# Kernel tuning notes

Hardware: AMD Instinct MI355X
Metric: run time of the kernel (lower is better)

The kernel has to match this reference:

```python
import jax, jax.numpy as jnp
import numpy as np

N = 200000   # active voxels
G = 128      # dense grid extent per axis
C = 128      # hidden channels
IN_C = 1
TEMB = 6
K = 27       # 3x3x3 kernel offsets


def _build_neighbors():
    # Sample N unique voxel coordinates in a G^3 grid and build the 27-offset
    # rulebook: neighbor_idx[k, i] = index of voxel at coord[i] + offset[k],
    # or N (sentinel -> zero-padded feature row) if inactive.
    rng = np.random.default_rng(0)
    lin = np.sort(rng.choice(G ** 3, size=N, replace=False)).astype(np.int64)
    x, r = lin // (G * G), lin % (G * G)
    y, z = r // G, r % G
    nidx = np.full((K, N), N, dtype=np.int32)
    k = 0
    for dx in (-1, 0, 1):
        for dy in (-1, 0, 1):
            for dz in (-1, 0, 1):
                nx, ny, nz = x + dx, y + dy, z + dz
                valid = (nx >= 0) & (nx < G) & (ny >= 0) & (ny < G) & (nz >= 0) & (nz < G)
                key = nx * (G * G) + ny * G + nz
                pos = np.searchsorted(lin, key)
                posc = np.clip(pos, 0, N - 1)
                found = valid & (lin[posc] == key)
                nidx[k] = np.where(found, posc, N).astype(np.int32)
                k += 1
    return jnp.asarray(nidx)


def setup_inputs() -> dict:
    key = jax.random.key(0)
    ks = jax.random.split(key, 8)
    s = jnp.float32(0.05)
    return {
        "features": jax.random.normal(ks[0], (N, IN_C), jnp.float32),
        "t": jax.random.randint(ks[1], (N,), 0, 1000, jnp.int32),
        "neighbor_idx": _build_neighbors(),
        "W1": jax.random.normal(ks[2], (K, IN_C + TEMB, C), jnp.float32) * s,
        "b1": jnp.zeros((C,), jnp.float32),
        "W2": jax.random.normal(ks[3], (K, C, C), jnp.float32) * s,
        "b2": jnp.zeros((C,), jnp.float32),
        "W3": jax.random.normal(ks[4], (C, C), jnp.float32) * s,
        "b3": jnp.zeros((C,), jnp.float32),
        "W4": jax.random.normal(ks[5], (C, 1), jnp.float32) * s,
        "b4": jnp.zeros((1,), jnp.float32),
    }


def _sinusoidal(t, dim):
    half = dim // 2
    freqs = (2.0 ** jnp.arange(half, dtype=jnp.float32)) * jnp.pi  # 2^k * pi
    ang = t.astype(jnp.float32)[:, None] * freqs[None, :]
    return jnp.concatenate([jnp.sin(ang), jnp.cos(ang)], -1)  # [N, dim]


def _sparse_conv3(x, W, b, nidx):
    # Submanifold sparse 3x3x3 conv: for each of 27 offsets, gather neighbor
    # features (zero row for missing) and accumulate a [Cin,Cout] matmul.
    xpad = jnp.concatenate([x, jnp.zeros((1, x.shape[1]), x.dtype)], 0)  # sentinel row
    acc0 = jnp.zeros((x.shape[0], W.shape[-1]), x.dtype)

    def step(acc, kw):
        idx, Wk = kw
        return acc + xpad[idx] @ Wk, None

    acc, _ = jax.lax.scan(step, acc0, (nidx, W))
    return acc + b


def reference(features, t, neighbor_idx, W1, b1, W2, b2, W3, b3, W4, b4):
    # time-embedding concat  [N, 1+6]
    x = jnp.concatenate([features, _sinusoidal(t, TEMB)], -1)
    # SparseConv3d(k=3) + Dropout(eval: identity) + SiLU
    h = jax.nn.silu(_sparse_conv3(x, W1, b1, neighbor_idx))
    h = jax.nn.silu(_sparse_conv3(h, W2, b2, neighbor_idx))
    # SparseConv3d(k=1) + SiLU  == pointwise matmul
    h = jax.nn.silu(h @ W3 + b3)
    # final 1x1 conv to out_channels=1
    return h @ W4 + b4
```

## Files before the change

kernel.cpp:

```cpp
#include <hip/hip_runtime.h>
#include <math.h>

#define N_VOX 200000
#define CCH   128
#define KOFF  27

typedef __attribute__((ext_vector_type(8))) short bf16x8;
typedef __attribute__((ext_vector_type(4))) float f32x4;

__device__ __forceinline__ float silu_f(float x) {
    return x / (1.0f + expf(-x));
}
__device__ __forceinline__ unsigned short f2bf(float x) {
    unsigned int u = __float_as_uint(x);
    u = (u + 0x7FFFu + ((u >> 16) & 1u)) >> 16;
    return (unsigned short)u;
}
__device__ __forceinline__ int xcd_swz(int orig, int nwg) {
    int q = nwg >> 3, r = nwg & 7;
    int xcd = orig & 7, pos = orig >> 3;
    return (xcd < r ? xcd * (q + 1) : r * (q + 1) + (xcd - r) * q) + pos;
}
__device__ __forceinline__ void gload_lds16(const void* g, void* l) {
    __builtin_amdgcn_global_load_lds(
        (const __attribute__((address_space(1))) unsigned int*)g,
        (__attribute__((address_space(3))) unsigned int*)l, 16, 0, 0);
}

__global__ void embed_kernel(const float* __restrict__ feat,
                             const int* __restrict__ t,
                             unsigned short* __restrict__ xeb) {
    int i = blockIdx.x * blockDim.x + threadIdx.x;
    if (i > N_VOX) return;
    union { unsigned short u[8]; int4 v; } o;
    if (i == N_VOX) {
        o.v = make_int4(0, 0, 0, 0);
    } else {
        o.u[0] = f2bf(feat[i]);
        float tf = (float)t[i];
#pragma unroll
        for (int kk = 0; kk < 3; ++kk) {
            float freq = (float)M_PI * (float)(1 << kk);
            float ang = tf * freq;
            o.u[1 + kk] = f2bf(sinf(ang));
            o.u[4 + kk] = f2bf(cosf(ang));
        }
        o.u[7] = 0;
    }
    *(int4*)(xeb + (size_t)i * 8) = o.v;
}

__global__ void convert_w1(const float* __restrict__ W1,
                           unsigned short* __restrict__ W1f) {
    int g = blockIdx.x * 256 + threadIdx.x;
    if (g >= 7 * 8 * 64) return;
    int l = g & 63;
    int rest = g >> 6;
    int nf = rest & 7;
    int kk = rest >> 3;
    int o = kk * 4 + (l >> 4);
    int co = nf * 16 + (l & 15);
    union { unsigned short u[8]; int4 v; } out;
#pragma unroll
    for (int j = 0; j < 8; ++j) {
        float w = 0.f;
        if (o < KOFF && j < 7) w = W1[((size_t)o * 7 + j) * CCH + co];
        out.u[j] = f2bf(w);
    }
    *(int4*)(W1f + (size_t)g * 8) = out.v;
}

__global__ void convert_w2(const float* __restrict__ W2,
                           unsigned short* __restrict__ W2f) {
    int g = blockIdx.x * 256 + threadIdx.x;
    int l = g & 63;
    int rest = g >> 6;
    int nf = rest & 7;
    int kkk = rest >> 3;
    int k = kkk >> 2, kk = kkk & 3;
    int ci0 = kk * 32 + (l >> 4) * 8;
    int co = nf * 16 + (l & 15);
    union { unsigned short u[8]; int4 v; } out;
#pragma unroll
    for (int j = 0; j < 8; ++j)
        out.u[j] = f2bf(W2[((size_t)k * CCH + ci0 + j) * CCH + co]);
    *(int4*)(W2f + (size_t)g * 8) = out.v;
}

__global__ void convert_w3(const float* __restrict__ W3,
                           unsigned short* __restrict__ W3f) {
    int g = blockIdx.x * 256 + threadIdx.x;
    if (g >= 4 * 8 * 64) return;
    int l = g & 63;
    int rest = g >> 6;
    int nf = rest & 7;
    int kk = rest >> 3;
    int ci0 = kk * 32 + (l >> 4) * 8;
    int co = nf * 16 + (l & 15);
    union { unsigned short u[8]; int4 v; } out;
#pragma unroll
    for (int j = 0; j < 8; ++j)
        out.u[j] = f2bf(W3[(size_t)(ci0 + j) * CCH + co]);
    *(int4*)(W3f + (size_t)g * 8) = out.v;
}

__global__ __launch_bounds__(256) void conv1_mfma(
    const unsigned short* __restrict__ xeb, const int* __restrict__ nidx,
    const unsigned short* __restrict__ W1f, const float* __restrict__ b1,
    unsigned short* __restrict__ h1b) {
    __shared__ int4 bufmem[2048];
    __shared__ int idxAll[128 * 28];

    int tid = threadIdx.x;
    int l = tid & 63, w = tid >> 6;
    int mw = w >> 1, nwv = w & 1;
    int wg = xcd_swz(blockIdx.x, gridDim.x);
    int v0 = wg * 128;

    for (int g = tid; g < KOFF * 128; g += 256) {
        int k = g >> 7, vi = g & 127;
        int v = v0 + vi;
        idxAll[vi * 28 + k] = (v < N_VOX) ? nidx[(size_t)k * N_VOX + v] : N_VOX;
    }
    if (tid < 128) idxAll[tid * 28 + 27] = N_VOX;
    __syncthreads();

    f32x4 acc[4][4];
#pragma unroll
    for (int m = 0; m < 4; ++m)
#pragma unroll
        for (int n = 0; n < 4; ++n) acc[m][n] = (f32x4)0.f;

    {
        int4 g0[2]; int rr[2], cc[2];
#pragma unroll
        for (int u = 0; u < 2; ++u) {
            int q = u * 256 + tid;
            int r = q >> 2, oo = q & 3;
            int idx = idxAll[r * 28 + oo];
            g0[u] = *(const int4*)(xeb + (size_t)idx * 8);
            rr[u] = r; cc[u] = oo ^ (r & 3);
        }
#pragma unroll
        for (int u = 0; u < 2; ++u) bufmem[rr[u] * 5 + cc[u]] = g0[u];
    }
    __syncthreads();

    for (int kk = 0; kk < 7; ++kk) {
        int cur = kk & 1;
        int4 gg[2]; int rr[2], cc[2];
        if (kk < 6) {
#pragma unroll
            for (int u = 0; u < 2; ++u) {
                int q = u * 256 + tid;
                int r = q >> 2, oo = q & 3;
                int idx = idxAll[r * 28 + (kk + 1) * 4 + oo];
                gg[u] = *(const int4*)(xeb + (size_t)idx * 8);
                rr[u] = r; cc[u] = oo ^ (r & 3);
            }
        }
        bf16x8 a[4], b[4];
#pragma unroll
        for (int n = 0; n < 4; ++n) {
            int nf = nwv * 4 + n;
            b[n] = *(const bf16x8*)(W1f + ((size_t)(kk * 8 + nf) * 64 + l) * 8);
        }
#pragma unroll
        for (int m = 0; m < 4; ++m) {
            int r = mw * 64 + m * 16 + (l & 15);
            int c = l >> 4;
            a[m] = *(const bf16x8*)&bufmem[cur * 640 + r * 5 + (c ^ (r & 3))];
        }
#pragma unroll
        for (int m = 0; m < 4; ++m)
#pragma unroll
            for (int n = 0; n < 4; ++n)
                acc[m][n] = __builtin_amdgcn_mfma_f32_16x16x32_bf16(
                    a[m], b[n], acc[m][n], 0, 0, 0);
        if (kk < 6) {
#pragma unroll
            for (int u = 0; u < 2; ++u)
                bufmem[(cur ^ 1) * 640 + rr[u] * 5 + cc[u]] = gg[u];
        }
        __syncthreads();
    }

    float bias[4];
#pragma unroll
    for (int n = 0; n < 4; ++n) bias[n] = b1[nwv * 64 + n * 16 + (l & 15)];
    unsigned short* H16 = (unsigned short*)bufmem;
#pragma unroll
    for (int m = 0; m < 4; ++m) {
        int rbase = mw * 64 + m * 16 + (l >> 4) * 4;
#pragma unroll
        for (int n = 0; n < 4; ++n) {
            int ch = nwv * 64 + n * 16 + (l & 15);
            int c = ch >> 3;
            f32x4 d = acc[m][n];
#pragma unroll
            for (int ri = 0; ri < 4; ++ri) {
                int r = rbase + ri;
                int s = (c & 8) | ((c & 7) ^ (r & 7));
                H16[r * 128 + s * 8 + (ch & 7)] = f2bf(silu_f(d[ri] + bias[n]));
            }
        }
    }
    __syncthreads();
#pragma unroll
    for (int u = 0; u < 8; ++u) {
        int q = u * 256 + tid;
        int r = q >> 4, s = q & 15;
        int c = (s & 8) | ((s & 7) ^ (r & 7));
        int v = v0 + r;
        if (v < N_VOX)
            *(int4*)(h1b + (size_t)v * CCH + c * 8) = bufmem[r * 16 + s];
    }
    if (blockIdx.x == 0 && tid < 16)
        *(int4*)(h1b + (size_t)N_VOX * CCH + tid * 8) = make_int4(0, 0, 0, 0);
}

#define STAGE3(bufsel, kq) {                                               \
    int _c = (w << 2) + (l >> 4);                                          \
    _Pragma("unroll") for (int _u = 0; _u < 8; ++_u) {                     \
        int _r = _u * 16 + (l & 15);                                       \
        int _idx = idxAll[(kq) * 128 + _r];                                \
        gload_lds16((const char*)h1b + ((size_t)_idx << 8) + (_c << 4),    \
                    (void*)&Abuf[bufsel][_u * 256 + tid]);                 \
    }                                                                      \
}

#define LOADB2(dst, kq, kh) {                                              \
    const unsigned short* _wb = W2f + (size_t)(kq) * 16384;                \
    _Pragma("unroll") for (int _j = 0; _j < 2; ++_j)                       \
        _Pragma("unroll") for (int _n = 0; _n < 4; ++_n)                   \
            dst[_j][_n] = *(const bf16x8*)(_wb +                           \
                ((size_t)(((kh)*2 + _j) * 8 + nwv * 4 + _n) * 64 + l) * 8);\
}

#define MPH(cur, kk, br) {                                                 \
    bf16x8 _a[4];                                                          \
    _Pragma("unroll") for (int _m = 0; _m < 4; ++_m)                       \
        _a[_m] = *(const bf16x8*)                                          \
            &Abuf[cur][(((mw * 4 + _m) * 4 + (kk)) << 6) + l];             \
    _Pragma("unroll") for (int _m = 0; _m < 4; ++_m)                       \
        _Pragma("unroll") for (int _n = 0; _n < 4; ++_n)                   \
            acc[_m][_n] = __builtin_amdgcn_mfma_f32_16x16x32_bf16(         \
                _a[_m], br[_n], acc[_m][_n], 0, 0, 0);                     \
}

#define STEP(KQ, BCUR, BNXT) {                                             \
    int _cur = (KQ) & 1, _nxt = _cur ^ 1;                                  \
    STAGE3(_nxt, (KQ) + 1);                                                \
    __builtin_amdgcn_sched_barrier(0);                                     \
    bf16x8 b23[2][4];                                                      \
    LOADB2(b23, (KQ), 1);                                                  \
    LOADB2(BNXT, (KQ) + 1, 0);                                             \
    __builtin_amdgcn_sched_barrier(0);                                     \
    MPH(_cur, 0, BCUR[0]);                                                 \
    MPH(_cur, 1, BCUR[1]);                                                 \
    MPH(_cur, 2, b23[0]);                                                  \
    MPH(_cur, 3, b23[1]);                                                  \
    asm volatile("s_waitcnt vmcnt(8)" ::: "memory");                       \
    __builtin_amdgcn_s_barrier();                                          \
}

__global__ __launch_bounds__(256, 2) void conv2_mfma(
    const unsigned short* __restrict__ h1b, const int* __restrict__ nidx,
    const unsigned short* __restrict__ W2f, const float* __restrict__ b2,
    const unsigned short* __restrict__ W3f, const float* __restrict__ b3,
    const float* __restrict__ W4, const float* __restrict__ b4,
    float* __restrict__ out) {
    __shared__ int4 Abuf[2][2048];
    __shared__ int idxAll[KOFF * 128];

    int tid = threadIdx.x;
    int l = tid & 63, w = tid >> 6;
    int mw = w >> 1, nwv = w & 1;
    int wg = xcd_swz(blockIdx.x, gridDim.x);
    int v0 = wg * 128;

    for (int g = tid; g < KOFF * 128; g += 256) {
        int k = g >> 7, vi = g & 127;
        int v = v0 + vi;
        idxAll[k * 128 + vi] = (v < N_VOX) ? nidx[(size_t)k * N_VOX + v] : N_VOX;
    }
    __syncthreads();

    f32x4 acc[4][4];
#pragma unroll
    for (int m = 0; m < 4; ++m)
#pragma unroll
        for (int n = 0; n < 4; ++n) acc[m][n] = (f32x4)0.f;

    bf16x8 bE[2][4], bO[2][4];

    STAGE3(0, 0);
    __builtin_amdgcn_sched_barrier(0);
    LOADB2(bE, 0, 0);
    __builtin_amdgcn_sched_barrier(0);
    asm volatile("s_waitcnt vmcnt(8)" ::: "memory");
    __builtin_amdgcn_s_barrier();

    for (int kp = 0; kp < 26; kp += 2) {
        STEP(kp, bE, bO);
        STEP(kp + 1, bO, bE);
    }
    {
        bf16x8 b23[2][4];
        LOADB2(b23, 26, 1);
        MPH(0, 0, bE[0]);
        MPH(0, 1, bE[1]);
        MPH(0, 2, b23[0]);
        MPH(0, 3, b23[1]);
    }
    __syncthreads();

    float bias2[4];
#pragma unroll
    for (int n = 0; n < 4; ++n) bias2[n] = b2[nwv * 64 + n * 16 + (l & 15)];
    unsigned short* H16 = (unsigned short*)&Abuf[0][0];
#pragma unroll
    for (int m = 0; m < 4; ++m) {
        int rbase = mw * 64 + m * 16 + (l >> 4) * 4;
#pragma unroll
        for (int n = 0; n < 4; ++n) {
            int ch = nwv * 64 + n * 16 + (l & 15);
            int c = ch >> 3;
            f32x4 d = acc[m][n];
#pragma unroll
            for (int ri = 0; ri < 4; ++ri) {
                int r = rbase + ri;
                int s = (c & 8) | ((c & 7) ^ (r & 7));
                H16[r * 128 + s * 8 + (ch & 7)] = f2bf(silu_f(d[ri] + bias2[n]));
            }
        }
    }
    __syncthreads();

    f32x4 p[4][4];
#pragma unroll
    for (int m = 0; m < 4; ++m)
#pragma unroll
        for (int n = 0; n < 4; ++n) p[m][n] = (f32x4)0.f;
#pragma unroll
    for (int kk = 0; kk < 4; ++kk) {
        bf16x8 a[4], b[4];
#pragma unroll
        for (int n = 0; n < 4; ++n) {
            int nf = nwv * 4 + n;
            b[n] = *(const bf16x8*)(W3f + ((size_t)(kk * 8 + nf) * 64 + l) * 8);
        }
#pragma unroll
        for (int m = 0; m < 4; ++m) {
            int r = mw * 64 + m * 16 + (l & 15);
            int c = kk * 4 + (l >> 4);
            int s = (c & 8) | ((c & 7) ^ (r & 7));
            a[m] = *(const bf16x8*)&H16[r * 128 + s * 8];
        }
#pragma unroll
        for (int m = 0; m < 4; ++m)
#pragma unroll
            for (int n = 0; n < 4; ++n)
                p[m][n] = __builtin_amdgcn_mfma_f32_16x16x32_bf16(
                    a[m], b[n], p[m][n], 0, 0, 0);
    }

    float w4v[4], b3v[4];
#pragma unroll
    for (int n = 0; n < 4; ++n) {
        int ch = nwv * 64 + n * 16 + (l & 15);
        w4v[n] = W4[ch];
        b3v[n] = b3[ch];
    }
    float* Osum = (float*)idxAll;
#pragma unroll
    for (int m = 0; m < 4; ++m) {
        float po[4] = {0.f, 0.f, 0.f, 0.f};
#pragma unroll
        for (int n = 0; n < 4; ++n) {
            f32x4 d = p[m][n];
#pragma unroll
            for (int ri = 0; ri < 4; ++ri)
                po[ri] += silu_f(d[ri] + b3v[n]) * w4v[n];
        }
#pragma unroll
        for (int off = 1; off < 16; off <<= 1)
#pragma unroll
            for (int ri = 0; ri < 4; ++ri)
                po[ri] += __shfl_xor(po[ri], off, 64);
        if ((l & 15) == 0) {
            int rbase = mw * 64 + m * 16 + (l >> 4) * 4;
#pragma unroll
            for (int ri = 0; ri < 4; ++ri)
                Osum[nwv * 128 + rbase + ri] = po[ri];
        }
    }
    __syncthreads();
    if (tid < 128) {
        int v = v0 + tid;
        if (v < N_VOX) out[v] = Osum[tid] + Osum[128 + tid] + b4[0];
    }
}

extern "C" void kernel_launch(void* const* d_in, const int* in_sizes, int n_in,
                              void* d_out, int out_size, void* d_ws,
                              size_t ws_size, hipStream_t stream) {
    const float* feat = (const float*)d_in[0];
    const int* t      = (const int*)d_in[1];
    const int* nidx   = (const int*)d_in[2];
    const float* W1   = (const float*)d_in[3];
    const float* b1   = (const float*)d_in[4];
    const float* W2   = (const float*)d_in[5];
    const float* b2   = (const float*)d_in[6];
    const float* W3   = (const float*)d_in[7];
    const float* b3   = (const float*)d_in[8];
    const float* W4   = (const float*)d_in[9];
    const float* b4   = (const float*)d_in[10];
    float* out = (float*)d_out;

    char* ws = (char*)d_ws;
    size_t off = 0;
    unsigned short* xeb = (unsigned short*)(ws + off);
    off += ((size_t)(N_VOX + 1) * 8 * 2 + 255) & ~(size_t)255;
    unsigned short* h1b = (unsigned short*)(ws + off);
    off += ((size_t)(N_VOX + 1) * CCH * 2 + 255) & ~(size_t)255;
    unsigned short* W1f = (unsigned short*)(ws + off);
    off += ((size_t)7 * 8 * 64 * 8 * 2 + 255) & ~(size_t)255;
    unsigned short* W2f = (unsigned short*)(ws + off);
    off += ((size_t)KOFF * 4 * 8 * 64 * 8 * 2 + 255) & ~(size_t)255;
    unsigned short* W3f = (unsigned short*)(ws + off);

    int grid1 = (N_VOX + 127) / 128;
    int grid2 = (N_VOX + 127) / 128;
    embed_kernel<<<(N_VOX + 1 + 255) / 256, 256, 0, stream>>>(feat, t, xeb);
    convert_w1<<<(7 * 8 * 64 + 255) / 256, 256, 0, stream>>>(W1, W1f);
    convert_w2<<<(KOFF * 4 * 8 * 64) / 256, 256, 0, stream>>>(W2, W2f);
    convert_w3<<<(4 * 8 * 64 + 255) / 256, 256, 0, stream>>>(W3, W3f);
    conv1_mfma<<<grid1, 256, 0, stream>>>(xeb, nidx, W1f, b1, h1b);
    conv2_mfma<<<grid2, 256, 0, stream>>>(h1b, nidx, W2f, b2, W3f, b3, W4, b4, out);
}
```

Baseline: 303.4 us.

## Double conv2 voxel tile to 256 with half-K pipeline steps and streamed indices

Each conv2 block now processes 256 voxels instead of 128, so each wave accumulates a 128x64 output tile and every W2 fragment fetched from global memory feeds twice as many MFMAs. Each 3x3x3 offset is split into two 64-channel half-steps, double-buffered in LDS. Neighbor indices are streamed into a small two-slot buffer instead of preloading all 27 offsets, which frees LDS for the larger A buffers. MFMA bursts get raised wave priority. In exchange, the accumulator array doubles, raising register pressure and spill risk under launch_bounds(256,2). The full vmcnt(0) wait each step may also expose more load latency.

```diff
diff --git a/kernel.cpp b/kernel.cpp
--- a/kernel.cpp
+++ b/kernel.cpp
@@ -219,48 +219,58 @@
         *(int4*)(h1b + (size_t)N_VOX * CCH + tid * 8) = make_int4(0, 0, 0, 0);
 }
 
-#define STAGE3(bufsel, kq) {                                               \
-    int _c = (w << 2) + (l >> 4);                                          \
+#define STAGE_S(buf, sq, ib) {                                             \
     _Pragma("unroll") for (int _u = 0; _u < 8; ++_u) {                     \
-        int _r = _u * 16 + (l & 15);                                       \
-        int _idx = idxAll[(kq) * 128 + _r];                                \
-        gload_lds16((const char*)h1b + ((size_t)_idx << 8) + (_c << 4),    \
-                    (void*)&Abuf[bufsel][_u * 256 + tid]);                 \
+        int _q = _u * 256 + tid;                                           \
+        int _row = ((_q >> 7) << 4) | (_q & 15);                           \
+        int _hi = (_q >> 4) & 3;                                           \
+        int _kk = (_q >> 6) & 1;                                           \
+        int _idx = idxbuf[ib][_row];                                       \
+        gload_lds16((const char*)h1b + ((size_t)(unsigned)_idx << 8) +     \
+                        ((sq) & 1) * 128 + _kk * 64 + _hi * 16,            \
+                    (void*)&Abuf[buf][_q]);                                \
     }                                                                      \
 }
 
-#define LOADB2(dst, kq, kh) {                                              \
-    const unsigned short* _wb = W2f + (size_t)(kq) * 16384;                \
-    _Pragma("unroll") for (int _j = 0; _j < 2; ++_j)                       \
+#define LOADB_S(dst, sq) {                                                 \
+    const unsigned short* _wb = W2f + (size_t)((sq) >> 1) * 16384 +        \
+                                (size_t)((sq) & 1) * 2 * 4096;             \
+    _Pragma("unroll") for (int _kk = 0; _kk < 2; ++_kk)                    \
         _Pragma("unroll") for (int _n = 0; _n < 4; ++_n)                   \
-            dst[_j][_n] = *(const bf16x8*)(_wb +                           \
-                ((size_t)(((kh)*2 + _j) * 8 + nwv * 4 + _n) * 64 + l) * 8);\
-}
-
-#define MPH(cur, kk, br) {                                                 \
-    bf16x8 _a[4];                                                          \
-    _Pragma("unroll") for (int _m = 0; _m < 4; ++_m)                       \
-        _a[_m] = *(const bf16x8*)                                          \
-            &Abuf[cur][(((mw * 4 + _m) * 4 + (kk)) << 6) + l];             \
-    _Pragma("unroll") for (int _m = 0; _m < 4; ++_m)                       \
-        _Pragma("unroll") for (int _n = 0; _n < 4; ++_n)                   \
-            acc[_m][_n] = __builtin_amdgcn_mfma_f32_16x16x32_bf16(         \
-                _a[_m], br[_n], acc[_m][_n], 0, 0, 0);                     \
-}
-
-#define STEP(KQ, BCUR, BNXT) {                                             \
-    int _cur = (KQ) & 1, _nxt = _cur ^ 1;                                  \
-    STAGE3(_nxt, (KQ) + 1);                                                \
+            dst[_kk][_n] = *(const bf16x8*)(_wb +                          \
+                ((size_t)(_kk * 8 + nwv * 4 + _n) * 64 + l) * 8);          \
+}
+
+#define MFMA_S(cur, bfr) {                                                 \
+    _Pragma("unroll") for (int _kk = 0; _kk < 2; ++_kk) {                  \
+        bf16x8 _a[8];                                                      \
+        _Pragma("unroll") for (int _m = 0; _m < 8; ++_m) {                 \
+            int _R = mw * 8 + _m;                                          \
+            _a[_m] = *(const bf16x8*)&Abuf[cur][((_R * 2 + _kk) << 6) + l];\
+        }                                                                  \
+        __builtin_amdgcn_s_setprio(1);                                     \
+        _Pragma("unroll") for (int _m = 0; _m < 8; ++_m)                   \
+            _Pragma("unroll") for (int _n = 0; _n < 4; ++_n)               \
+                acc[_m][_n] = __builtin_amdgcn_mfma_f32_16x16x32_bf16(     \
+                    _a[_m], bfr[_kk][_n], acc[_m][_n], 0, 0, 0);           \
+        __builtin_amdgcn_s_setprio(0);                                     \
+    }                                                                      \
+}
+
+#define STEP_S(SQ, CUR, DO_STAGE, DO_IDX) {                                \
+    bf16x8 bfr[2][4];                                                      \
+    LOADB_S(bfr, SQ);                                                      \
     __builtin_amdgcn_sched_barrier(0);                                     \
-    bf16x8 b23[2][4];                                                      \
-    LOADB2(b23, (KQ), 1);                                                  \
-    LOADB2(BNXT, (KQ) + 1, 0);                                             \
+    if (DO_STAGE) { STAGE_S((CUR) ^ 1, (SQ) + 1, ((((SQ) + 1) >> 1) & 1)); }\
+    if (DO_IDX) {                                                          \
+        int _k1 = ((SQ) >> 1) + 1;                                         \
+        int _v = v0 + tid;                                                 \
+        idxbuf[_k1 & 1][tid] =                                             \
+            (_v < N_VOX) ? nidx[(size_t)_k1 * N_VOX + _v] : N_VOX;         \
+    }                                                                      \
     __builtin_amdgcn_sched_barrier(0);                                     \
-    MPH(_cur, 0, BCUR[0]);                                                 \
-    MPH(_cur, 1, BCUR[1]);                                                 \
-    MPH(_cur, 2, b23[0]);                                                  \
-    MPH(_cur, 3, b23[1]);                                                  \
-    asm volatile("s_waitcnt vmcnt(8)" ::: "memory");                       \
+    MFMA_S(CUR, bfr);                                                      \
+    asm volatile("s_waitcnt vmcnt(0)" ::: "memory");                       \
     __builtin_amdgcn_s_barrier();                                          \
 }
 
@@ -271,57 +281,48 @@
     const float* __restrict__ W4, const float* __restrict__ b4,
     float* __restrict__ out) {
     __shared__ int4 Abuf[2][2048];
-    __shared__ int idxAll[KOFF * 128];
+    __shared__ int idxbuf[2][256];
+    __shared__ float Osum[512];
 
     int tid = threadIdx.x;
     int l = tid & 63, w = tid >> 6;
     int mw = w >> 1, nwv = w & 1;
     int wg = xcd_swz(blockIdx.x, gridDim.x);
-    int v0 = wg * 128;
-
-    for (int g = tid; g < KOFF * 128; g += 256) {
-        int k = g >> 7, vi = g & 127;
-        int v = v0 + vi;
-        idxAll[k * 128 + vi] = (v < N_VOX) ? nidx[(size_t)k * N_VOX + v] : N_VOX;
-    }
-    __syncthreads();
-
-    f32x4 acc[4][4];
-#pragma unroll
-    for (int m = 0; m < 4; ++m)
+    int v0 = wg * 256;
+
+    f32x4 acc[8][4];
+#pragma unroll
+    for (int m = 0; m < 8; ++m)
 #pragma unroll
         for (int n = 0; n < 4; ++n) acc[m][n] = (f32x4)0.f;
 
-    bf16x8 bE[2][4], bO[2][4];
-
-    STAGE3(0, 0);
-    __builtin_amdgcn_sched_barrier(0);
-    LOADB2(bE, 0, 0);
-    __builtin_amdgcn_sched_barrier(0);
-    asm volatile("s_waitcnt vmcnt(8)" ::: "memory");
-    __builtin_amdgcn_s_barrier();
-
-    for (int kp = 0; kp < 26; kp += 2) {
-        STEP(kp, bE, bO);
-        STEP(kp + 1, bO, bE);
-    }
     {
-        bf16x8 b23[2][4];
-        LOADB2(b23, 26, 1);
-        MPH(0, 0, bE[0]);
-        MPH(0, 1, bE[1]);
-        MPH(0, 2, b23[0]);
-        MPH(0, 3, b23[1]);
-    }
-    __syncthreads();
+        int v = v0 + tid;
+        idxbuf[0][tid] = (v < N_VOX) ? nidx[v] : N_VOX;
+    }
+    __syncthreads();
+    STAGE_S(0, 0, 0);
+    {
+        int v = v0 + tid;
+        idxbuf[1][tid] = (v < N_VOX) ? nidx[(size_t)N_VOX + v] : N_VOX;
+    }
+    asm volatile("s_waitcnt vmcnt(0)" ::: "memory");
+    __syncthreads();
+
+    for (int sp = 0; sp < 52; sp += 2) {
+        STEP_S(sp, 0, true, ((sp >> 1) + 1 < KOFF));
+        STEP_S(sp + 1, 1, true, false);
+    }
+    STEP_S(52, 0, true, false);
+    STEP_S(53, 1, false, false);
 
     float bias2[4];
 #pragma unroll
     for (int n = 0; n < 4; ++n) bias2[n] = b2[nwv * 64 + n * 16 + (l & 15)];
     unsigned short* H16 = (unsigned short*)&Abuf[0][0];
 #pragma unroll
-    for (int m = 0; m < 4; ++m) {
-        int rbase = mw * 64 + m * 16 + (l >> 4) * 4;
+    for (int m = 0; m < 8; ++m) {
+        int rbase = mw * 128 + m * 16 + (l >> 4) * 4;
 #pragma unroll
         for (int n = 0; n < 4; ++n) {
             int ch = nwv * 64 + n * 16 + (l & 15);
@@ -337,28 +338,28 @@
     }
     __syncthreads();
 
-    f32x4 p[4][4];
-#pragma unroll
-    for (int m = 0; m < 4; ++m)
+    f32x4 p[8][4];
+#pragma unroll
+    for (int m = 0; m < 8; ++m)
 #pragma unroll
         for (int n = 0; n < 4; ++n) p[m][n] = (f32x4)0.f;
 #pragma unroll
     for (int kk = 0; kk < 4; ++kk) {
-        bf16x8 a[4], b[4];
+        bf16x8 a[8], b[4];
 #pragma unroll
         for (int n = 0; n < 4; ++n) {
             int nf = nwv * 4 + n;
             b[n] = *(const bf16x8*)(W3f + ((size_t)(kk * 8 + nf) * 64 + l) * 8);
         }
 #pragma unroll
-        for (int m = 0; m < 4; ++m) {
-            int r = mw * 64 + m * 16 + (l & 15);
+        for (int m = 0; m < 8; ++m) {
+            int r = mw * 128 + m * 16 + (l & 15);
             int c = kk * 4 + (l >> 4);
             int s = (c & 8) | ((c & 7) ^ (r & 7));
             a[m] = *(const bf16x8*)&H16[r * 128 + s * 8];
         }
 #pragma unroll
-        for (int m = 0; m < 4; ++m)
+        for (int m = 0; m < 8; ++m)
 #pragma unroll
             for (int n = 0; n < 4; ++n)
                 p[m][n] = __builtin_amdgcn_mfma_f32_16x16x32_bf16(
@@ -372,9 +373,8 @@
         w4v[n] = W4[ch];
         b3v[n] = b3[ch];
     }
-    float* Osum = (float*)idxAll;
-#pragma unroll
-    for (int m = 0; m < 4; ++m) {
+#pragma unroll
+    for (int m = 0; m < 8; ++m) {
         float po[4] = {0.f, 0.f, 0.f, 0.f};
 #pragma unroll
         for (int n = 0; n < 4; ++n) {
@@ -389,16 +389,16 @@
             for (int ri = 0; ri < 4; ++ri)
                 po[ri] += __shfl_xor(po[ri], off, 64);
         if ((l & 15) == 0) {
-            int rbase = mw * 64 + m * 16 + (l >> 4) * 4;
+            int rbase = mw * 128 + m * 16 + (l >> 4) * 4;
 #pragma unroll
             for (int ri = 0; ri < 4; ++ri)
-                Osum[nwv * 128 + rbase + ri] = po[ri];
-        }
-    }
-    __syncthreads();
-    if (tid < 128) {
+                Osum[nwv * 256 + rbase + ri] = po[ri];
+        }
+    }
+    __syncthreads();
+    {
         int v = v0 + tid;
-        if (v < N_VOX) out[v] = Osum[tid] + Osum[128 + tid] + b4[0];
+        if (v < N_VOX) out[v] = Osum[tid] + Osum[256 + tid] + b4[0];
     }
 }
 
@@ -427,11 +427,11 @@
     unsigned short* W1f = (unsigned short*)(ws + off);
     off += ((size_t)7 * 8 * 64 * 8 * 2 + 255) & ~(size_t)255;
     unsigned short* W2f = (unsigned short*)(ws + off);
-    off += ((size_t)KOFF * 4 * 8 * 64 * 8 * 2 + 255) & ~(size_t)255;
+    off += ((size_t)(KOFF + 1) * 4 * 8 * 64 * 8 * 2 + 255) & ~(size_t)255;
     unsigned short* W3f = (unsigned short*)(ws + off);
 
     int grid1 = (N_VOX + 127) / 128;
-    int grid2 = (N_VOX + 127) / 128;
+    int grid2 = (N_VOX + 255) / 256;
     embed_kernel<<<(N_VOX + 1 + 255) / 256, 256, 0, stream>>>(feat, t, xeb);
     convert_w1<<<(7 * 8 * 64 + 255) / 256, 256, 0, stream>>>(W1, W1f);
     convert_w2<<<(KOFF * 4 * 8 * 64) / 256, 256, 0, stream>>>(W2, W2f);
```

Result: faster. 277.3 us (-8.6%).
